# Performance work log

Hardware: AMD Instinct MI355X
Metric: run time of the kernel (lower is better)

The kernel has to match this reference:

```python
import jax, jax.numpy as jnp
import numpy as np

N, E, MUL, NZ, NR = 8192, 65536, 64, 10, 8
SQ3 = 3.0 ** 0.5
SQ2 = 2.0 ** 0.5


def _mlp(x, ws):
    # e3nn FullyConnectedNet: no biases, 1/sqrt(fan_in) scaling, silu on hidden layers
    for i, w in enumerate(ws):
        x = x @ w / jnp.sqrt(jnp.float32(w.shape[0]))
        if i < len(ws) - 1:
            x = jax.nn.silu(x)
    return x


def setup_inputs() -> dict:
    key = jax.random.key(0)
    ks = jax.random.split(key, 20)
    g = lambda i, sh: jax.random.normal(ks[i], sh, dtype=jnp.float32)
    return dict(
        node_attrs=jax.random.uniform(ks[0], (N, NZ), dtype=jnp.float32),
        node_feats=g(1, (N, MUL * 4)),            # 64x0e + 64x1o
        edge_attrs=g(2, (E, 4)),                  # SH: 1x0e + 1x1o
        edge_feats=g(3, (E, NR)),                 # radial basis
        edge_index=jax.random.randint(ks[4], (2, E), 0, N),
        magmom_node_inv_feats=g(5, (N, NR)),
        magmom_node_attrs=g(6, (N, 4)),           # 1x0e + 1x1o
        W_up_s=g(7, (MUL, MUL)), W_up_v=g(8, (MUL, MUL)),
        rmlp_w0=g(9, (2 * NR, 64)), rmlp_w1=g(10, (64, 64)),
        rmlp_w2=g(11, (64, 64)), rmlp_w3=g(12, (64, 5 * MUL)),
        mag_w=g(13, (2 * NR, 13 * MUL)),
        dens_w=g(14, (NR, 1)),
        lin_s_w=g(15, (5 * MUL, MUL)), lin_v_w=g(16, (8 * MUL, MUL)),
        skip_w_s=g(17, (MUL, NZ, MUL)), skip_w_v=g(18, (MUL, NZ, MUL)),
    )


def reference(node_attrs, node_feats, edge_attrs, edge_feats, edge_index,
              magmom_node_inv_feats, magmom_node_attrs,
              W_up_s, W_up_v, rmlp_w0, rmlp_w1, rmlp_w2, rmlp_w3,
              mag_w, dens_w, lin_s_w, lin_v_w, skip_w_s, skip_w_v):
    sender, receiver = edge_index[0], edge_index[1]
    num_nodes = node_feats.shape[0]
    mul = W_up_s.shape[0]

    # linear_up (per-l channel mixing)
    s = node_feats[:, :mul]
    v = node_feats[:, mul:].reshape(num_nodes, mul, 3)
    s = (s @ W_up_s) / jnp.sqrt(jnp.float32(mul))
    v = jnp.einsum('nui,uw->nwi', v, W_up_v) / jnp.sqrt(jnp.float32(mul))

    # radial weights conditioned on edge feats + sender magmom invariants
    efm = jnp.concatenate([edge_feats, magmom_node_inv_feats[sender]], axis=-1)
    tp_w = _mlp(efm, [rmlp_w0, rmlp_w1, rmlp_w2, rmlp_w3]).reshape(-1, 5, mul)
    wm = (efm @ mag_w / jnp.sqrt(jnp.float32(mag_w.shape[0]))).reshape(-1, 13, mul)
    edge_density = jnp.tanh((edge_feats @ dens_w / jnp.sqrt(jnp.float32(NR))) ** 2)  # [E,1]

    # conv_tp: node_feats[sender] x edge SH, uvu with per-edge weights (5 paths)
    xs, xv = s[sender], v[sender]          # [E,mul], [E,mul,3]
    y0, y1 = edge_attrs[:, :1], edge_attrs[:, 1:]
    m_s0 = tp_w[:, 0] * xs * y0                                       # 0e x 0e -> 0e
    m_v0 = tp_w[:, 1, :, None] * xs[:, :, None] * y1[:, None, :]      # 0e x 1o -> 1o
    m_v1 = tp_w[:, 2, :, None] * xv * y0[:, :, None]                  # 1o x 0e -> 1o
    m_s1 = tp_w[:, 3] * jnp.einsum('eui,ei->eu', xv, y1) / SQ3        # 1o x 1o -> 0e
    m_v2 = tp_w[:, 4, :, None] * jnp.cross(xv, y1[:, None, :]) / SQ2  # 1o x 1o -> 1e

    # magmom_conv_tp: mji x magmom_node_attrs[sender], uvu (13 paths)
    ma = magmom_node_attrs[sender]
    m0, m1 = ma[:, :1], ma[:, 1:]
    out_s, out_v = [], []
    p = 0
    for ss in (m_s0, m_s1):
        out_s.append(wm[:, p] * ss * m0); p += 1
        out_v.append(wm[:, p, :, None] * ss[:, :, None] * m1[:, None, :]); p += 1
    for vv in (m_v0, m_v1, m_v2):
        out_v.append(wm[:, p, :, None] * vv * m0[:, :, None]); p += 1
        out_s.append(wm[:, p] * jnp.einsum('eui,ei->eu', vv, m1) / SQ3); p += 1
        out_v.append(wm[:, p, :, None] * jnp.cross(vv, m1[:, None, :]) / SQ2); p += 1
    mm_s = jnp.stack(out_s, axis=1)   # [E,5,mul]
    mm_v = jnp.stack(out_v, axis=1)   # [E,8,mul,3]

    # scatter-sum to receivers
    density = jax.ops.segment_sum(edge_density, receiver, num_segments=num_nodes)  # [N,1]
    ms = jax.ops.segment_sum(mm_s, receiver, num_segments=num_nodes)               # [N,5,mul]
    mv = jax.ops.segment_sum(mm_v, receiver, num_segments=num_nodes)               # [N,8,mul,3]

    # magmom_linear + density normalization
    ms = ms.reshape(num_nodes, 5 * mul) @ lin_s_w / jnp.sqrt(jnp.float32(5 * mul))
    mv = jnp.einsum('nui,uw->nwi', mv.reshape(num_nodes, 8 * mul, 3), lin_v_w) / jnp.sqrt(jnp.float32(8 * mul))
    ms = ms / (density + 1.0)
    mv = mv / (density[:, :, None] + 1.0)

    # skip FullyConnectedTensorProduct with scalar node_attrs (species one-hot)
    fan = jnp.sqrt(jnp.float32(skip_w_s.shape[0] * skip_w_s.shape[1]))
    o_s = jnp.einsum('nu,nv,uvw->nw', ms, node_attrs, skip_w_s) / fan
    o_v = jnp.einsum('nui,nv,uvw->nwi', mv, node_attrs, skip_w_v) / fan

    # reshape_irreps: [N, mul, 1+3]
    return jnp.concatenate([o_s[:, :, None], o_v], axis=-1)
```

## Files before the change

### kernel.cpp

```cpp
#include <hip/hip_runtime.h>
#include <hip/hip_bf16.h>

#define NN 8192
#define EE 65536

typedef unsigned short u16;
typedef __attribute__((ext_vector_type(8))) short bf16x8;
typedef __attribute__((ext_vector_type(8))) unsigned short u16x8;
typedef __attribute__((ext_vector_type(4))) float f32x4;

#define OFF_W0    0
#define OFF_W1    2048
#define OFF_W2    6144
#define OFF_W3M   10240
#define OFF_MAGB  59392
#define OFF_LINS  79872
#define OFF_LINV  100352
#define OFF_SKS   133120
#define OFF_SKV   174080
#define WT_TOTAL  215040

__device__ __forceinline__ u16 f2bf(float f) {
  __hip_bfloat16 h = __float2bfloat16(f);
  return *reinterpret_cast<u16*>(&h);
}
__device__ __forceinline__ float bf2f(u16 v) {
  union { unsigned int u; float f; } x; x.u = ((unsigned int)v) << 16; return x.f;
}
__device__ __forceinline__ void split2(float x, u16& h, u16& l) {
  __hip_bfloat16 bh = __float2bfloat16(x);
  h = *reinterpret_cast<u16*>(&bh);
  float r = x - __bfloat162float(bh);
  __hip_bfloat16 bl = __float2bfloat16(r);
  l = *reinterpret_cast<u16*>(&bl);
}

#define MFMA(a, b, c) __builtin_amdgcn_mfma_f32_16x16x32_bf16((a), (b), (c), 0, 0, 0)

__global__ __launch_bounds__(256, 4) void k_edge(
    const u16* __restrict__ efm_h, const u16* __restrict__ efm_l,
    const u16* __restrict__ wt_h, const u16* __restrict__ wt_l,
    u16* __restrict__ cmbP)
{
  __shared__ u16 Hh[64 * 72], Hl[64 * 72];
  __shared__ u16 Bs[2][3072];
  __shared__ u16 Ct[64 * 80];
  const int tid  = threadIdx.x;
  const size_t pos0 = (size_t)blockIdx.x * 64;
  const int wave = tid >> 6, lane = tid & 63;
  const int quad = lane >> 4, lrow = lane & 15;
  const int kbase = quad * 8;
  const int rw = wave * 16;

  bf16x8 eah = {}, eal = {};
  if (quad < 2) {
    eah = *reinterpret_cast<const bf16x8*>(&efm_h[(pos0 + rw + lrow) * 16 + kbase]);
    eal = *reinterpret_cast<const bf16x8*>(&efm_l[(pos0 + rw + lrow) * 16 + kbase]);
  }

  {
    #pragma unroll
    for (int nt = 0; nt < 4; ++nt) {
      const size_t bo = (size_t)nt * 512 + lane * 8;
      const bf16x8 fbh = *reinterpret_cast<const bf16x8*>(wt_h + OFF_W0 + bo);
      const bf16x8 fbl = *reinterpret_cast<const bf16x8*>(wt_l + OFF_W0 + bo);
      f32x4 acc = {};
      acc = MFMA(eah, fbh, acc); acc = MFMA(eah, fbl, acc); acc = MFMA(eal, fbh, acc);
      #pragma unroll
      for (int r = 0; r < 4; ++r) {
        float t = acc[r];
        t = t / (1.0f + __expf(-t));
        u16 hh, ll; split2(t, hh, ll);
        const int row = rw + quad * 4 + r, col = nt * 16 + lrow;
        Hh[row * 72 + col] = hh; Hl[row * 72 + col] = ll;
      }
    }
  }

  #pragma unroll
  for (int layer = 0; layer < 2; ++layer) {
    const int OFF = layer ? OFF_W2 : OFF_W1;
    bf16x8 fah[2], fal[2];
    #pragma unroll
    for (int ks = 0; ks < 2; ++ks) {
      fah[ks] = *reinterpret_cast<const bf16x8*>(&Hh[(rw + lrow) * 72 + ks * 32 + kbase]);
      fal[ks] = *reinterpret_cast<const bf16x8*>(&Hl[(rw + lrow) * 72 + ks * 32 + kbase]);
    }
    f32x4 acc[4] = {};
    #pragma unroll
    for (int nt = 0; nt < 4; ++nt)
      #pragma unroll
      for (int ks = 0; ks < 2; ++ks) {
        const size_t bo = (size_t)(nt * 2 + ks) * 512 + lane * 8;
        const bf16x8 fbh = *reinterpret_cast<const bf16x8*>(wt_h + OFF + bo);
        const bf16x8 fbl = *reinterpret_cast<const bf16x8*>(wt_l + OFF + bo);
        acc[nt] = MFMA(fah[ks], fbh, acc[nt]);
        acc[nt] = MFMA(fah[ks], fbl, acc[nt]);
        acc[nt] = MFMA(fal[ks], fbh, acc[nt]);
      }
    #pragma unroll
    for (int nt = 0; nt < 4; ++nt)
      #pragma unroll
      for (int r = 0; r < 4; ++r) {
        float t = acc[nt][r];
        t = t / (1.0f + __expf(-t));
        u16 hh, ll; split2(t, hh, ll);
        const int row = rw + quad * 4 + r, col = nt * 16 + lrow;
        Hh[row * 72 + col] = hh; Hl[row * 72 + col] = ll;
      }
  }

  unsigned int tp[5][4][2];

  auto STORE_P = [&](u16* dst) {
    #pragma unroll
    for (int i = 0; i < 2; ++i) {
      const int idx = lane + i * 64;
      const int rl = idx >> 3, c2 = idx & 7;
      const uint4 v4 = *reinterpret_cast<const uint4*>(
          &Ct[(rw + rl) * 80 + ((c2 * 8) ^ (((rl >> 2) & 3) << 4))]);
      *reinterpret_cast<uint4*>(&dst[(pos0 + rw + rl) * 64 + c2 * 8]) = v4;
    }
  };

  {
    bf16x8 fah[3], fal[3];
    #pragma unroll
    for (int ks = 0; ks < 2; ++ks) {
      fah[ks] = *reinterpret_cast<const bf16x8*>(&Hh[(rw + lrow) * 72 + ks * 32 + kbase]);
      fal[ks] = *reinterpret_cast<const bf16x8*>(&Hl[(rw + lrow) * 72 + ks * 32 + kbase]);
    }
    fah[2] = eah; fal[2] = eal;

    auto STAGE_A = [&](int s, int buf) {
      const size_t src = (size_t)OFF_W3M + (size_t)s * 1536;
      #pragma unroll
      for (int i = 0; i < 2; ++i) {
        const int idx = tid + i * 256;
        if (idx < 384) {
          const int b = (idx >= 192);
          const int off = (idx - (b ? 192 : 0)) * 8;
          *reinterpret_cast<uint4*>(&Bs[buf][(b ? 1536 : 0) + off]) =
              *reinterpret_cast<const uint4*>((b ? wt_l : wt_h) + src + off);
        }
      }
    };

    STAGE_A(0, 0);
    #pragma unroll
    for (int s = 0; s < 32; ++s) {
      __syncthreads();
      if (s + 1 < 32) STAGE_A(s + 1, (s + 1) & 1);
      const int nt = s & 3, g = s >> 2;
      f32x4 acc = {};
      #pragma unroll
      for (int ks = 0; ks < 3; ++ks) {
        const bf16x8 bh = *reinterpret_cast<const bf16x8*>(&Bs[s & 1][ks * 512 + lane * 8]);
        const bf16x8 bl = *reinterpret_cast<const bf16x8*>(&Bs[s & 1][1536 + ks * 512 + lane * 8]);
        acc = MFMA(fah[ks], bh, acc); acc = MFMA(fah[ks], bl, acc); acc = MFMA(fal[ks], bh, acc);
      }
      if (g < 5) {
        tp[g][nt][0] = (unsigned)f2bf(acc[0]) | ((unsigned)f2bf(acc[1]) << 16);
        tp[g][nt][1] = (unsigned)f2bf(acc[2]) | ((unsigned)f2bf(acc[3]) << 16);
      } else {
        const int q = (g == 7) ? 3 : 0;
        #pragma unroll
        for (int r = 0; r < 4; ++r) {
          const float tv = bf2f((u16)((tp[q][nt][r >> 1] >> ((r & 1) * 16)) & 0xffffu));
          Ct[(rw + quad * 4 + r) * 80 + ((nt * 16 + lrow) ^ (quad << 4))] = f2bf(acc[r] * tv);
        }
        if (nt == 3) STORE_P(cmbP + (size_t)(g - 5) * ((size_t)EE * 64));
      }
    }
  }

  {
    auto STAGE_B = [&](int t, int buf) {
      const size_t src = (size_t)OFF_MAGB + (size_t)t * 512;
      if (tid < 128) {
        const int b = (tid >= 64);
        const int off = (tid - (b ? 64 : 0)) * 8;
        *reinterpret_cast<uint4*>(&Bs[buf][(b ? 1536 : 0) + off]) =
            *reinterpret_cast<const uint4*>((b ? wt_l : wt_h) + src + off);
      }
    };

    STAGE_B(0, 0);
    #pragma unroll
    for (int t = 0; t < 40; ++t) {
      __syncthreads();
      if (t + 1 < 40) STAGE_B(t + 1, (t + 1) & 1);
      const int nt = t & 3, p = t >> 2;
      constexpr int QB[10] = {3, 1, 1, 1, 2, 2, 2, 4, 4, 4};
      const int q = QB[p];
      const bf16x8 bh = *reinterpret_cast<const bf16x8*>(&Bs[t & 1][lane * 8]);
      const bf16x8 bl = *reinterpret_cast<const bf16x8*>(&Bs[t & 1][1536 + lane * 8]);
      f32x4 acc = {};
      acc = MFMA(eah, bh, acc); acc = MFMA(eah, bl, acc); acc = MFMA(eal, bh, acc);
      #pragma unroll
      for (int r = 0; r < 4; ++r) {
        const float tv = bf2f((u16)((tp[q][nt][r >> 1] >> ((r & 1) * 16)) & 0xffffu));
        Ct[(rw + quad * 4 + r) * 80 + ((nt * 16 + lrow) ^ (quad << 4))] = f2bf(acc[r] * tv);
      }
      if (nt == 3) STORE_P(cmbP + (size_t)(3 + p) * ((size_t)EE * 64));
    }
  }
}

template<int RT, int OUT, bool SILU, int DDIV>
__global__ __launch_bounds__(256) void k_mgemm(
    const u16* __restrict__ X1h, const u16* __restrict__ X1l, int x1rs, int K1,
    const u16* __restrict__ X2h, const u16* __restrict__ X2l, int x2rs, int K2,
    const u16* __restrict__ Wth, const u16* __restrict__ Wtl, int K,
    void* __restrict__ O1, void* __restrict__ O2, int ors,
    const float* __restrict__ dens)
{
  constexpr int NTN = (RT == 128) ? 4 : 1;
  constexpr int AIT = RT * 8 / 256;
  __shared__ u16 Ah[RT * 40];
  __shared__ u16 Al[RT * 40];
  __shared__ u16 Bh[64 * 40];
  __shared__ u16 Bl[64 * 40];
  const int tid  = threadIdx.x;
  const int row0 = blockIdx.x * RT;
  const int col0 = blockIdx.y * 64;
  const int wave = tid >> 6, lane = tid & 63;
  const int quad = lane >> 4, lrow = lane & 15;
  const int kbase = quad * 8;
  const int rw  = (RT == 128) ? wave * 32 : 0;
  const int ntb = (RT == 128) ? 0 : wave;

  f32x4 acc[2][NTN] = {};

  for (int k0 = 0; k0 < K; k0 += 32) {
    #pragma unroll
    for (int i = 0; i < AIT; ++i) {
      const int idx = tid + i * 256;
      const int b = idx / (RT * 4), rc = idx & (RT * 4 - 1);
      const int r = rc >> 2, c = rc & 3;
      const int gk = k0 + c * 8;
      uint4 v = make_uint4(0u, 0u, 0u, 0u);
      if (gk < K1)
        v = *reinterpret_cast<const uint4*>(&(b ? X1l : X1h)[(size_t)(row0 + r) * x1rs + gk]);
      else if (gk - K1 < K2)
        v = *reinterpret_cast<const uint4*>(&(b ? X2l : X2h)[(size_t)(row0 + r) * x2rs + gk - K1]);
      *reinterpret_cast<uint4*>(&(b ? Al : Ah)[r * 40 + c * 8]) = v;
    }
    #pragma unroll
    for (int i = 0; i < 2; ++i) {
      const int idx = tid + i * 256;
      const int b = idx >> 8, rc = idx & 255;
      const int n = rc >> 2, c = rc & 3;
      const uint4 v = *reinterpret_cast<const uint4*>(
          &(b ? Wtl : Wth)[(size_t)(col0 + n) * K + k0 + c * 8]);
      *reinterpret_cast<uint4*>(&(b ? Bl : Bh)[n * 40 + c * 8]) = v;
    }
    __syncthreads();

    bf16x8 fah[2], fal[2], fbh[NTN], fbl[NTN];
    #pragma unroll
    for (int mt = 0; mt < 2; ++mt) {
      const int ro = (rw + mt * 16 + lrow) * 40 + kbase;
      fah[mt] = *reinterpret_cast<const bf16x8*>(&Ah[ro]);
      fal[mt] = *reinterpret_cast<const bf16x8*>(&Al[ro]);
    }
    #pragma unroll
    for (int nt = 0; nt < NTN; ++nt) {
      const int ro = ((ntb + nt) * 16 + lrow) * 40 + kbase;
      fbh[nt] = *reinterpret_cast<const bf16x8*>(&Bh[ro]);
      fbl[nt] = *reinterpret_cast<const bf16x8*>(&Bl[ro]);
    }
    #pragma unroll
    for (int mt = 0; mt < 2; ++mt)
      #pragma unroll
      for (int nt = 0; nt < NTN; ++nt) {
        acc[mt][nt] = MFMA(fah[mt], fbh[nt], acc[mt][nt]);
        acc[mt][nt] = MFMA(fah[mt], fbl[nt], acc[mt][nt]);
        acc[mt][nt] = MFMA(fal[mt], fbh[nt], acc[mt][nt]);
      }
    __syncthreads();
  }

  #pragma unroll
  for (int mt = 0; mt < 2; ++mt)
    #pragma unroll
    for (int nt = 0; nt < NTN; ++nt)
      #pragma unroll
      for (int r = 0; r < 4; ++r) {
        const int grow = row0 + rw + mt * 16 + quad * 4 + r;
        const int gcol = col0 + (ntb + nt) * 16 + lrow;
        float t = acc[mt][nt][r];
        if (SILU) t = t / (1.0f + __expf(-t));
        if (DDIV > 0) t *= 1.0f / (dens[grow / DDIV] + 1.0f);
        const size_t oi = (size_t)grow * ors + gcol;
        if (OUT == 0) {
          reinterpret_cast<float*>(O1)[oi] = t;
        } else if (OUT == 1) {
          u16 hh, ll;
          split2(t, hh, ll);
          reinterpret_cast<u16*>(O1)[oi] = hh;
          reinterpret_cast<u16*>(O2)[oi] = ll;
        } else {
          reinterpret_cast<u16*>(O1)[oi] = f2bf(t);
        }
      }
}

__global__ __launch_bounds__(256) void k_skipm(
    const float* __restrict__ ms2, const float* __restrict__ mv2,
    const float* __restrict__ na,
    const u16* __restrict__ wt_h, const u16* __restrict__ wt_l,
    float* __restrict__ out)
{
  __shared__ u16 Ah[32 * 40];
  __shared__ u16 Al[32 * 40];
  __shared__ u16 Bh[64 * 40];
  __shared__ u16 Bl[64 * 40];
  const int tid  = threadIdx.x;
  const bool isv = blockIdx.x >= (NN / 32);
  const int row0 = (isv ? (blockIdx.x - NN / 32) : blockIdx.x) * 32;
  const float* C = isv ? mv2 : ms2;
  const u16* Bth = wt_h + (isv ? OFF_SKV : OFF_SKS);
  const u16* Btl = wt_l + (isv ? OFF_SKV : OFF_SKS);
  const int wave = tid >> 6, lane = tid & 63;
  const int quad = lane >> 4, lrow = lane & 15;
  const int kbase = quad * 8;

  f32x4 acc[2] = {};

  for (int k0 = 0; k0 < 640; k0 += 32) {
    #pragma unroll
    for (int i = 0; i < 4; ++i) {
      const int e = tid + i * 256;
      const int r = e >> 5, kk = e & 31;
      const int k = k0 + kk;
      const int u = k / 10, v = k - u * 10;
      const int row = row0 + r;
      const int n = isv ? (row / 3) : row;
      const float t = C[(size_t)row * 64 + u] * na[n * 10 + v];
      u16 hh, ll;
      split2(t, hh, ll);
      Ah[r * 40 + kk] = hh;
      Al[r * 40 + kk] = ll;
    }
    #pragma unroll
    for (int i = 0; i < 2; ++i) {
      const int idx = tid + i * 256;
      const int b = idx >> 8, rc = idx & 255;
      const int nw = rc >> 2, c = rc & 3;
      const uint4 v4 = *reinterpret_cast<const uint4*>(
          &(b ? Btl : Bth)[(size_t)nw * 640 + k0 + c * 8]);
      *reinterpret_cast<uint4*>(&(b ? Bl : Bh)[nw * 40 + c * 8]) = v4;
    }
    __syncthreads();

    bf16x8 fah[2], fal[2], fbh, fbl;
    #pragma unroll
    for (int mt = 0; mt < 2; ++mt) {
      const int ro = (mt * 16 + lrow) * 40 + kbase;
      fah[mt] = *reinterpret_cast<const bf16x8*>(&Ah[ro]);
      fal[mt] = *reinterpret_cast<const bf16x8*>(&Al[ro]);
    }
    {
      const int ro = (wave * 16 + lrow) * 40 + kbase;
      fbh = *reinterpret_cast<const bf16x8*>(&Bh[ro]);
      fbl = *reinterpret_cast<const bf16x8*>(&Bl[ro]);
    }
    #pragma unroll
    for (int mt = 0; mt < 2; ++mt) {
      acc[mt] = MFMA(fah[mt], fbh, acc[mt]);
      acc[mt] = MFMA(fah[mt], fbl, acc[mt]);
      acc[mt] = MFMA(fal[mt], fbh, acc[mt]);
    }
    __syncthreads();
  }

  #pragma unroll
  for (int mt = 0; mt < 2; ++mt)
    #pragma unroll
    for (int r = 0; r < 4; ++r) {
      const int row = row0 + mt * 16 + quad * 4 + r;
      const int w = wave * 16 + lrow;
      if (isv) {
        const int n = row / 3, i = row - n * 3;
        out[(size_t)n * 256 + w * 4 + 1 + i] = acc[mt][r];
      } else {
        out[(size_t)row * 256 + w * 4] = acc[mt][r];
      }
    }
}

template<int RT>
__global__ __launch_bounds__(256) void k_gemm(
    const float* __restrict__ X, int xrs, int xes, int xco, int xcob,
    const float* __restrict__ W, int K, int NOUT,
    float scale, float* __restrict__ OUTp, int ors, int oob)
{
  constexpr int RPT = RT / 16;
  __shared__ float Xs[RT * 65];
  __shared__ float Ws[64 * 64];
  const int tid  = threadIdx.x;
  const int row0 = blockIdx.x * RT;
  const int col0 = blockIdx.y * 64;
  const int z    = blockIdx.z;
  const int xc   = xco + z * xcob;
  const int oo   = z * oob;
  const int ci = tid & 15;
  const int ri = tid >> 4;
  float acc[RPT][4] = {};

  for (int k0 = 0; k0 < K; k0 += 64) {
    const int kc  = (K - k0 >= 64) ? 64 : (K - k0);
    const int ksh = (kc == 64) ? 6 : 4;
    for (int idx = tid; idx < kc * RT; idx += 256) {
      const int r = idx >> ksh, kk = idx & (kc - 1);
      Xs[r * 65 + kk] = X[(size_t)(row0 + r) * xrs + xc + (size_t)(k0 + kk) * xes];
    }
    for (int idx = tid; idx < (kc << 6); idx += 256) {
      const int kk = idx >> 6, c = idx & 63;
      Ws[kk * 64 + c] = W[(size_t)(k0 + kk) * NOUT + col0 + c];
    }
    __syncthreads();
    for (int kk = 0; kk < kc; ++kk) {
      const float4 wv = *reinterpret_cast<const float4*>(&Ws[kk * 64 + ci * 4]);
      #pragma unroll
      for (int j = 0; j < RPT; ++j) {
        const float x = Xs[(ri * RPT + j) * 65 + kk];
        acc[j][0] += x * wv.x; acc[j][1] += x * wv.y;
        acc[j][2] += x * wv.z; acc[j][3] += x * wv.w;
      }
    }
    __syncthreads();
  }

  #pragma unroll
  for (int j = 0; j < RPT; ++j) {
    const int row = row0 + ri * RPT + j;
    *reinterpret_cast<float4*>(OUTp + (size_t)row * ors + oo + col0 + ci * 4) =
        make_float4(acc[j][0] * scale, acc[j][1] * scale, acc[j][2] * scale, acc[j][3] * scale);
  }
}

__global__ __launch_bounds__(256) void k_count(const int* __restrict__ rcv, int* __restrict__ counts) {
  const int e = blockIdx.x * 256 + threadIdx.x;
  atomicAdd(&counts[rcv[e]], 1);
}

__global__ __launch_bounds__(1024) void k_scan(const int* __restrict__ counts,
                                               int* __restrict__ offs, int* __restrict__ cursor) {
  __shared__ int part[1024];
  const int tid = threadIdx.x;
  int local[8];
  int s = 0;
  #pragma unroll
  for (int j = 0; j < 8; ++j) { local[j] = s; s += counts[tid * 8 + j]; }
  part[tid] = s;
  __syncthreads();
  for (int off = 1; off < 1024; off <<= 1) {
    int v = 0;
    if (tid >= off) v = part[tid - off];
    __syncthreads();
    part[tid] += v;
    __syncthreads();
  }
  const int base = part[tid] - s;
  #pragma unroll
  for (int j = 0; j < 8; ++j) {
    const int o = base + local[j];
    offs[tid * 8 + j] = o;
    cursor[tid * 8 + j] = o;
  }
  if (tid == 1023) offs[NN] = part[1023];
}

__global__ __launch_bounds__(256) void k_fill(const int* __restrict__ rcv,
                                              int* __restrict__ cursor, int* __restrict__ perm) {
  const int e = blockIdx.x * 256 + threadIdx.x;
  const int pos = atomicAdd(&cursor[rcv[e]], 1);
  perm[pos] = e;
}

__global__ __launch_bounds__(256) void k_permw(
    const float* __restrict__ w0, const float* __restrict__ w1,
    const float* __restrict__ w2, const float* __restrict__ w3,
    const float* __restrict__ mag_w, const float* __restrict__ lin_s,
    const float* __restrict__ lin_v, const float* __restrict__ skip_s,
    const float* __restrict__ skip_v,
    u16* __restrict__ wt_h, u16* __restrict__ wt_l)
{
  const int id = blockIdx.x * 256 + threadIdx.x;
  float val = 0.f;
  if (id < OFF_W1) {
    const int i = id - OFF_W0;
    const int tile = i >> 9, rem = i & 511, lane = rem >> 3, e = rem & 7;
    const int quad = lane >> 4, lrow = lane & 15;
    const int n = tile * 16 + lrow, k = quad * 8 + e;
    val = (k < 16) ? w0[k * 64 + n] * 0.25f : 0.f;
  } else if (id < OFF_W2) {
    const int i = id - OFF_W1;
    const int tile = i >> 9, rem = i & 511, lane = rem >> 3, e = rem & 7;
    const int quad = lane >> 4, lrow = lane & 15;
    const int n = (tile >> 1) * 16 + lrow, k = (tile & 1) * 32 + quad * 8 + e;
    val = w1[k * 64 + n] * 0.125f;
  } else if (id < OFF_W3M) {
    const int i = id - OFF_W2;
    const int tile = i >> 9, rem = i & 511, lane = rem >> 3, e = rem & 7;
    const int quad = lane >> 4, lrow = lane & 15;
    const int n = (tile >> 1) * 16 + lrow, k = (tile & 1) * 32 + quad * 8 + e;
    val = w2[k * 64 + n] * 0.125f;
  } else if (id < OFF_MAGB) {
    const int i = id - OFF_W3M;
    const int tile = i >> 9, rem = i & 511, lane = rem >> 3, e = rem & 7;
    const int quad = lane >> 4, lrow = lane & 15;
    const int gnt = tile / 3, ks = tile - gnt * 3;
    const int n = (gnt >> 2) * 64 + (gnt & 3) * 16 + lrow;
    const int k = ks * 32 + quad * 8 + e;
    if (n < 320) {
      val = (k < 64) ? w3[k * 320 + n] * 0.125f : 0.f;
    } else {
      const int p = (n - 320) >> 6, u = n & 63;
      val = (k >= 64 && k < 80) ? mag_w[(k - 64) * 832 + p * 64 + u] * 0.25f : 0.f;
    }
  } else if (id < OFF_LINS) {
    const int i = id - OFF_MAGB;
    const int tile = i >> 9, rem = i & 511, lane = rem >> 3, e = rem & 7;
    const int quad = lane >> 4, lrow = lane & 15;
    const int n = (tile >> 2) * 64 + (tile & 3) * 16 + lrow;
    const int k = quad * 8 + e;
    const int p = n >> 6, u = n & 63;
    val = (k < 16) ? mag_w[k * 832 + (3 + p) * 64 + u] * 0.25f : 0.f;
  } else if (id < OFF_LINV) {
    const int i = id - OFF_LINS, n = i / 320, k = i - n * 320;
    val = lin_s[k * 64 + n] * 0.05590169944f;
  } else if (id < OFF_SKS) {
    const int i = id - OFF_LINV, n = i >> 9, k = i & 511;
    val = lin_v[k * 64 + n] * 0.04419417382f;
  } else if (id < OFF_SKV) {
    const int i = id - OFF_SKS, w = i / 640, k = i - w * 640;
    val = skip_s[k * 64 + w] * 0.03952847075f;
  } else if (id < WT_TOTAL) {
    const int i = id - OFF_SKV, w = i / 640, k = i - w * 640;
    val = skip_v[k * 64 + w] * 0.03952847075f;
  } else {
    return;
  }
  u16 hh, ll;
  split2(val, hh, ll);
  wt_h[id] = hh;
  wt_l[id] = ll;
}

__global__ __launch_bounds__(256) void k_build(
    const int* __restrict__ perm, const int* __restrict__ snd,
    const float* __restrict__ edge_attrs, const float* __restrict__ edge_feats,
    const float* __restrict__ mm_inv, const float* __restrict__ dens_w,
    int* __restrict__ snd_perm, float* __restrict__ ya_perm,
    float* __restrict__ dq_perm, u16* __restrict__ efm_h, u16* __restrict__ efm_l)
{
  const int pos = blockIdx.x * 256 + threadIdx.x;
  const int e = perm[pos];
  const int s = snd[e];
  snd_perm[pos] = s;
  reinterpret_cast<float4*>(ya_perm)[pos] = reinterpret_cast<const float4*>(edge_attrs)[e];
  const float4 ef0 = reinterpret_cast<const float4*>(edge_feats)[e * 2];
  const float4 ef1 = reinterpret_cast<const float4*>(edge_feats)[e * 2 + 1];
  const float4 mi0 = reinterpret_cast<const float4*>(mm_inv)[s * 2];
  const float4 mi1 = reinterpret_cast<const float4*>(mm_inv)[s * 2 + 1];
  float q = ef0.x * dens_w[0] + ef0.y * dens_w[1] + ef0.z * dens_w[2] + ef0.w * dens_w[3]
          + ef1.x * dens_w[4] + ef1.y * dens_w[5] + ef1.z * dens_w[6] + ef1.w * dens_w[7];
  q *= 0.35355339059f;
  dq_perm[pos] = tanhf(q * q);
  float vals[16] = { ef0.x, ef0.y, ef0.z, ef0.w, ef1.x, ef1.y, ef1.z, ef1.w,
                     mi0.x, mi0.y, mi0.z, mi0.w, mi1.x, mi1.y, mi1.z, mi1.w };
  u16 hh[16], ll[16];
  #pragma unroll
  for (int i = 0; i < 16; ++i) split2(vals[i], hh[i], ll[i]);
  reinterpret_cast<uint4*>(&efm_h[(size_t)pos * 16])[0] = reinterpret_cast<uint4*>(hh)[0];
  reinterpret_cast<uint4*>(&efm_h[(size_t)pos * 16])[1] = reinterpret_cast<uint4*>(hh)[1];
  reinterpret_cast<uint4*>(&efm_l[(size_t)pos * 16])[0] = reinterpret_cast<uint4*>(ll)[0];
  reinterpret_cast<uint4*>(&efm_l[(size_t)pos * 16])[1] = reinterpret_cast<uint4*>(ll)[1];
}

__global__ __launch_bounds__(256) void k_gather(
    const int* __restrict__ snd_perm,
    const float* __restrict__ ya_perm,
    const float* __restrict__ dq_perm,
    const float* __restrict__ mm_attrs,
    const float* __restrict__ s_buf,
    const float* __restrict__ v_buf,
    const u16* __restrict__ cmbP,
    const int* __restrict__ offs,
    u16* __restrict__ ms_h, u16* __restrict__ ms_l,
    u16* __restrict__ mv_h, u16* __restrict__ mv_l,
    float* __restrict__ dens)
{
  __shared__ float red[2][30][64];
  const int tid  = threadIdx.x;
  const int lane = tid & 63;
  const int nib  = tid >> 7;
  const int half = (tid >> 6) & 1;
  const int n = blockIdx.x * 2 + nib;

  float acc_s[5] = {0.f, 0.f, 0.f, 0.f, 0.f};
  float acc_v[8][3] = {};
  float dacc = 0.f;
  const int start0 = offs[n], end0 = offs[n + 1];
  const int mid = start0 + ((end0 - start0 + 1) >> 1);
  const int start = half ? mid : start0;
  const int end   = half ? end0 : mid;

  int s_nx = 0;
  if (start < end) s_nx = snd_perm[start];
  for (int pos = start; pos < end; ++pos) {
    const int s = s_nx;
    if (pos + 1 < end) s_nx = snd_perm[pos + 1];

    const float4 ya = reinterpret_cast<const float4*>(ya_perm)[pos];
    const float4 mm = reinterpret_cast<const float4*>(mm_attrs)[s];
    dacc += dq_perm[pos];
    const float y0 = ya.x, y1x = ya.y, y1y = ya.z, y1z = ya.w;
    const float m0 = mm.x, m1x = mm.y, m1y = mm.z, m1z = mm.w;
    const float xs  = s_buf[s * 64 + lane];
    const float xvx = v_buf[(s * 3 + 0) * 64 + lane];
    const float xvy = v_buf[(s * 3 + 1) * 64 + lane];
    const float xvz = v_buf[(s * 3 + 2) * 64 + lane];

    float cp[13];
    #pragma unroll
    for (int p = 0; p < 13; ++p)
      cp[p] = bf2f(cmbP[(size_t)p * ((size_t)EE * 64) + (size_t)pos * 64 + lane]);

    const float gs0 = xs * y0;
    const float gd  = (xvx * y1x + xvy * y1y + xvz * y1z) * 0.57735026919f;
    const float g0x = xs * y1x, g0y = xs * y1y, g0z = xs * y1z;
    const float g1x = xvx * y0, g1y = xvy * y0, g1z = xvz * y0;
    const float g2x = (xvy * y1z - xvz * y1y) * 0.70710678119f;
    const float g2y = (xvz * y1x - xvx * y1z) * 0.70710678119f;
    const float g2z = (xvx * y1y - xvy * y1x) * 0.70710678119f;

    acc_s[0]    += cp[0] * gs0 * m0;
    acc_v[0][0] += cp[1] * gs0 * m1x; acc_v[0][1] += cp[1] * gs0 * m1y; acc_v[0][2] += cp[1] * gs0 * m1z;
    acc_s[1]    += cp[2] * gd * m0;
    acc_v[1][0] += cp[3] * gd * m1x; acc_v[1][1] += cp[3] * gd * m1y; acc_v[1][2] += cp[3] * gd * m1z;

#define VV_BLOCK(vx, vy, vz, cA, cB, cC, vslotA, sslot, vslotB)                           \
    acc_v[vslotA][0] += (cA) * (vx) * m0;                                                 \
    acc_v[vslotA][1] += (cA) * (vy) * m0;                                                 \
    acc_v[vslotA][2] += (cA) * (vz) * m0;                                                 \
    acc_s[sslot] += (cB) * ((vx) * m1x + (vy) * m1y + (vz) * m1z) * 0.57735026919f;       \
    {                                                                                     \
      const float ccx = (vy) * m1z - (vz) * m1y;                                          \
      const float ccy = (vz) * m1x - (vx) * m1z;                                          \
      const float ccz = (vx) * m1y - (vy) * m1x;                                          \
      acc_v[vslotB][0] += (cC) * ccx * 0.70710678119f;                                    \
      acc_v[vslotB][1] += (cC) * ccy * 0.70710678119f;                                    \
      acc_v[vslotB][2] += (cC) * ccz * 0.70710678119f;                                    \
    }

    VV_BLOCK(g0x, g0y, g0z, cp[4], cp[5], cp[6], 2, 2, 3)
    VV_BLOCK(g1x, g1y, g1z, cp[7], cp[8], cp[9], 4, 3, 5)
    VV_BLOCK(g2x, g2y, g2z, cp[10], cp[11], cp[12], 6, 4, 7)
#undef VV_BLOCK
  }

  if (half == 1) {
    #pragma unroll
    for (int j = 0; j < 5; ++j) red[nib][j][lane] = acc_s[j];
    #pragma unroll
    for (int p = 0; p < 8; ++p)
      #pragma unroll
      for (int i = 0; i < 3; ++i) red[nib][5 + p * 3 + i][lane] = acc_v[p][i];
    red[nib][29][lane] = dacc;
  }
  __syncthreads();
  if (half == 0) {
    #pragma unroll
    for (int j = 0; j < 5; ++j) acc_s[j] += red[nib][j][lane];
    #pragma unroll
    for (int p = 0; p < 8; ++p)
      #pragma unroll
      for (int i = 0; i < 3; ++i) acc_v[p][i] += red[nib][5 + p * 3 + i][lane];
    dacc += red[nib][29][lane];

    #pragma unroll
    for (int j = 0; j < 5; ++j) {
      u16 hh, ll;
      split2(acc_s[j], hh, ll);
      ms_h[(size_t)n * 320 + j * 64 + lane] = hh;
      ms_l[(size_t)n * 320 + j * 64 + lane] = ll;
    }
    #pragma unroll
    for (int p = 0; p < 8; ++p)
      #pragma unroll
      for (int i = 0; i < 3; ++i) {
        u16 hh, ll;
        split2(acc_v[p][i], hh, ll);
        mv_h[((size_t)n * 3 + i) * 512 + p * 64 + lane] = hh;
        mv_l[((size_t)n * 3 + i) * 512 + p * 64 + lane] = ll;
      }
    if (lane == 0) dens[n] = dacc;
  }
}

extern "C" void kernel_launch(void* const* d_in, const int* in_sizes, int n_in,
                              void* d_out, int out_size, void* d_ws, size_t ws_size,
                              hipStream_t stream)
{
  const float* node_attrs = (const float*)d_in[0];
  const float* node_feats = (const float*)d_in[1];
  const float* edge_attrs = (const float*)d_in[2];
  const float* edge_feats = (const float*)d_in[3];
  const int*   edge_index = (const int*)d_in[4];
  const float* mm_inv     = (const float*)d_in[5];
  const float* mm_attrs   = (const float*)d_in[6];
  const float* W_up_s     = (const float*)d_in[7];
  const float* W_up_v     = (const float*)d_in[8];
  const float* w0         = (const float*)d_in[9];
  const float* w1         = (const float*)d_in[10];
  const float* w2         = (const float*)d_in[11];
  const float* w3         = (const float*)d_in[12];
  const float* mag_w      = (const float*)d_in[13];
  const float* dens_w     = (const float*)d_in[14];
  const float* lin_s      = (const float*)d_in[15];
  const float* lin_v      = (const float*)d_in[16];
  const float* skip_s     = (const float*)d_in[17];
  const float* skip_v     = (const float*)d_in[18];
  float* out = (float*)d_out;

  char* wp = (char*)d_ws;
  auto alloc = [&](size_t b) { char* p = wp; wp += (b + 255) & ~(size_t)255; return p; };
  float* s_buf  = (float*)alloc((size_t)NN * 64 * 4);
  float* v_buf  = (float*)alloc((size_t)NN * 192 * 4);
  float* ya_p   = (float*)alloc((size_t)EE * 4 * 4);
  float* dq_p   = (float*)alloc((size_t)EE * 4);
  int*   snd_p  = (int*)alloc((size_t)EE * 4);
  u16*   efm_h  = (u16*)alloc((size_t)EE * 16 * 2);
  u16*   efm_l  = (u16*)alloc((size_t)EE * 16 * 2);
  u16*   hA_h   = (u16*)alloc((size_t)EE * 64 * 2);
  u16*   hA_l   = (u16*)alloc((size_t)EE * 64 * 2);
  u16*   hB_h   = (u16*)alloc((size_t)EE * 64 * 2);
  u16*   hB_l   = (u16*)alloc((size_t)EE * 64 * 2);
  u16*   cmbP   = (u16*)alloc((size_t)13 * EE * 64 * 2);
  u16*   mv_h   = (u16*)alloc((size_t)NN * 1536 * 2);
  u16*   mv_l   = (u16*)alloc((size_t)NN * 1536 * 2);
  float* dens   = (float*)alloc((size_t)NN * 4);
  int*   counts = (int*)alloc((size_t)NN * 4);
  int*   offs   = (int*)alloc((size_t)(NN + 1) * 4);
  int*   cursor = (int*)alloc((size_t)NN * 4);
  int*   perm   = (int*)alloc((size_t)EE * 4);
  u16*   wt_h   = (u16*)alloc((size_t)WT_TOTAL * 2);
  u16*   wt_l   = (u16*)alloc((size_t)WT_TOTAL * 2);
  u16*   ms_h   = hB_h;
  u16*   ms_l   = hB_l;
  float* ms2    = (float*)hA_h;
  float* mv2    = (float*)hA_l;

  const int* snd = edge_index;
  const int* rcv = edge_index + EE;

  hipMemsetAsync(counts, 0, (size_t)NN * 4, stream);
  k_count<<<EE / 256, 256, 0, stream>>>(rcv, counts);
  k_scan<<<1, 1024, 0, stream>>>(counts, offs, cursor);
  k_fill<<<EE / 256, 256, 0, stream>>>(rcv, cursor, perm);
  k_build<<<EE / 256, 256, 0, stream>>>(perm, snd, edge_attrs, edge_feats, mm_inv, dens_w,
                                        snd_p, ya_p, dq_p, efm_h, efm_l);
  k_permw<<<(WT_TOTAL + 255) / 256, 256, 0, stream>>>(w0, w1, w2, w3, mag_w, lin_s, lin_v,
                                                     skip_s, skip_v, wt_h, wt_l);

  k_gemm<32><<<dim3(NN / 32, 1, 1), 256, 0, stream>>>(
      node_feats, 256, 1, 0, 0, W_up_s, 64, 64, 0.125f, s_buf, 64, 0);
  k_gemm<32><<<dim3(NN / 32, 1, 3), 256, 0, stream>>>(
      node_feats, 256, 3, 64, 1, W_up_v, 64, 64, 0.125f, v_buf, 192, 64);

  k_edge<<<EE / 64, 256, 0, stream>>>(efm_h, efm_l, wt_h, wt_l, cmbP);

  k_gather<<<NN / 2, 256, 0, stream>>>(snd_p, ya_p, dq_p, mm_attrs,
                                       s_buf, v_buf, cmbP, offs,
                                       ms_h, ms_l, mv_h, mv_l, dens);

  k_mgemm<32, 0, false, 1><<<dim3(NN / 32, 1), 256, 0, stream>>>(
      ms_h, ms_l, 320, 320, nullptr, nullptr, 0, 0,
      wt_h + OFF_LINS, wt_l + OFF_LINS, 320, ms2, nullptr, 64, dens);
  k_mgemm<32, 0, false, 3><<<dim3(NN * 3 / 32, 1), 256, 0, stream>>>(
      mv_h, mv_l, 512, 512, nullptr, nullptr, 0, 0,
      wt_h + OFF_LINV, wt_l + OFF_LINV, 512, mv2, nullptr, 64, dens);

  k_skipm<<<NN / 32 + NN * 3 / 32, 256, 0, stream>>>(
      ms2, mv2, node_attrs, wt_h, wt_l, out);
}
```

Measured before the change: 296.5 us.

## Interleave radial and magmom GEMM phases to shrink tp register array

Merges the two GEMM phases (radial MLP last layer and magmom projection) into one table-driven loop over 18 product tiles. Each tp group is consumed right after it is computed, so only a 4x2 register buffer is kept instead of 5x4x2. This cuts register pressure and may raise occupancy. In exchange, the outer loop is no longer unrolled and uses runtime lookups in device constant tables, which adds branching and scalar loads.

```diff
diff --git a/kernel.cpp b/kernel.cpp
--- a/kernel.cpp
+++ b/kernel.cpp
@@ -19,6 +19,10 @@
 #define OFF_SKS   133120
 #define OFF_SKV   174080
 #define WT_TOTAL  215040
+
+__device__ const int PKIND[18] = {0,0,0, 0,0,1, 0,1,1,1, 0,1,1,1, 0,1,1,1};
+__device__ const int PTILE[18] = {0,5,6, 3,7,0, 1,1,2,3, 2,4,5,6, 4,7,8,9};
+__device__ const int PROLE[18] = {-1,0,1, -1,2,3, -1,4,5,6, -1,7,8,9, -1,10,11,12};
 
 __device__ __forceinline__ u16 f2bf(float f) {
   __hip_bfloat16 h = __float2bfloat16(f);
@@ -110,19 +114,6 @@
       }
   }
 
-  unsigned int tp[5][4][2];
-
-  auto STORE_P = [&](u16* dst) {
-    #pragma unroll
-    for (int i = 0; i < 2; ++i) {
-      const int idx = lane + i * 64;
-      const int rl = idx >> 3, c2 = idx & 7;
-      const uint4 v4 = *reinterpret_cast<const uint4*>(
-          &Ct[(rw + rl) * 80 + ((c2 * 8) ^ (((rl >> 2) & 3) << 4))]);
-      *reinterpret_cast<uint4*>(&dst[(pos0 + rw + rl) * 64 + c2 * 8]) = v4;
-    }
-  };
-
   {
     bf16x8 fah[3], fal[3];
     #pragma unroll
@@ -132,77 +123,77 @@
     }
     fah[2] = eah; fal[2] = eal;
 
-    auto STAGE_A = [&](int s, int buf) {
-      const size_t src = (size_t)OFF_W3M + (size_t)s * 1536;
-      #pragma unroll
-      for (int i = 0; i < 2; ++i) {
-        const int idx = tid + i * 256;
-        if (idx < 384) {
-          const int b = (idx >= 192);
-          const int off = (idx - (b ? 192 : 0)) * 8;
+    auto STAGE = [&](int pl, int nt, int buf) {
+      if (PKIND[pl]) {
+        const size_t src = (size_t)OFF_MAGB + (size_t)(PTILE[pl] * 4 + nt) * 512;
+        if (tid < 128) {
+          const int b = (tid >= 64);
+          const int off = (tid - (b ? 64 : 0)) * 8;
           *reinterpret_cast<uint4*>(&Bs[buf][(b ? 1536 : 0) + off]) =
               *reinterpret_cast<const uint4*>((b ? wt_l : wt_h) + src + off);
         }
+      } else {
+        const size_t src = (size_t)OFF_W3M + (size_t)(PTILE[pl] * 4 + nt) * 1536;
+        #pragma unroll
+        for (int i2 = 0; i2 < 2; ++i2) {
+          const int idx = tid + i2 * 256;
+          if (idx < 384) {
+            const int b = (idx >= 192);
+            const int off = (idx - (b ? 192 : 0)) * 8;
+            *reinterpret_cast<uint4*>(&Bs[buf][(b ? 1536 : 0) + off]) =
+                *reinterpret_cast<const uint4*>((b ? wt_l : wt_h) + src + off);
+          }
+        }
       }
     };
 
-    STAGE_A(0, 0);
-    #pragma unroll
-    for (int s = 0; s < 32; ++s) {
-      __syncthreads();
-      if (s + 1 < 32) STAGE_A(s + 1, (s + 1) & 1);
-      const int nt = s & 3, g = s >> 2;
-      f32x4 acc = {};
-      #pragma unroll
-      for (int ks = 0; ks < 3; ++ks) {
-        const bf16x8 bh = *reinterpret_cast<const bf16x8*>(&Bs[s & 1][ks * 512 + lane * 8]);
-        const bf16x8 bl = *reinterpret_cast<const bf16x8*>(&Bs[s & 1][1536 + ks * 512 + lane * 8]);
-        acc = MFMA(fah[ks], bh, acc); acc = MFMA(fah[ks], bl, acc); acc = MFMA(fal[ks], bh, acc);
-      }
-      if (g < 5) {
-        tp[g][nt][0] = (unsigned)f2bf(acc[0]) | ((unsigned)f2bf(acc[1]) << 16);
-        tp[g][nt][1] = (unsigned)f2bf(acc[2]) | ((unsigned)f2bf(acc[3]) << 16);
-      } else {
-        const int q = (g == 7) ? 3 : 0;
-        #pragma unroll
-        for (int r = 0; r < 4; ++r) {
-          const float tv = bf2f((u16)((tp[q][nt][r >> 1] >> ((r & 1) * 16)) & 0xffffu));
-          Ct[(rw + quad * 4 + r) * 80 + ((nt * 16 + lrow) ^ (quad << 4))] = f2bf(acc[r] * tv);
+    auto STORE_P = [&](u16* dst) {
+      #pragma unroll
+      for (int i = 0; i < 2; ++i) {
+        const int idx = lane + i * 64;
+        const int rl = idx >> 3, c2 = idx & 7;
+        const uint4 v4 = *reinterpret_cast<const uint4*>(
+            &Ct[(rw + rl) * 80 + ((c2 * 8) ^ (((rl >> 2) & 3) << 4))]);
+        *reinterpret_cast<uint4*>(&dst[(pos0 + rw + rl) * 64 + c2 * 8]) = v4;
+      }
+    };
+
+    unsigned int tp[4][2];
+    int buf = 0;
+    STAGE(0, 0, 0);
+    for (int pl = 0; pl < 18; ++pl) {
+      const int kind = PKIND[pl], role = PROLE[pl];
+      #pragma unroll
+      for (int nt = 0; nt < 4; ++nt) {
+        __syncthreads();
+        if (nt < 3) STAGE(pl, nt + 1, buf ^ 1);
+        else if (pl + 1 < 18) STAGE(pl + 1, 0, buf ^ 1);
+        f32x4 acc = {};
+        if (kind == 0) {
+          #pragma unroll
+          for (int ks = 0; ks < 3; ++ks) {
+            const bf16x8 bh = *reinterpret_cast<const bf16x8*>(&Bs[buf][ks * 512 + lane * 8]);
+            const bf16x8 bl = *reinterpret_cast<const bf16x8*>(&Bs[buf][1536 + ks * 512 + lane * 8]);
+            acc = MFMA(fah[ks], bh, acc); acc = MFMA(fah[ks], bl, acc); acc = MFMA(fal[ks], bh, acc);
+          }
+        } else {
+          const bf16x8 bh = *reinterpret_cast<const bf16x8*>(&Bs[buf][lane * 8]);
+          const bf16x8 bl = *reinterpret_cast<const bf16x8*>(&Bs[buf][1536 + lane * 8]);
+          acc = MFMA(fah[2], bh, acc); acc = MFMA(fah[2], bl, acc); acc = MFMA(fal[2], bh, acc);
         }
-        if (nt == 3) STORE_P(cmbP + (size_t)(g - 5) * ((size_t)EE * 64));
-      }
-    }
-  }
-
-  {
-    auto STAGE_B = [&](int t, int buf) {
-      const size_t src = (size_t)OFF_MAGB + (size_t)t * 512;
-      if (tid < 128) {
-        const int b = (tid >= 64);
-        const int off = (tid - (b ? 64 : 0)) * 8;
-        *reinterpret_cast<uint4*>(&Bs[buf][(b ? 1536 : 0) + off]) =
-            *reinterpret_cast<const uint4*>((b ? wt_l : wt_h) + src + off);
-      }
-    };
-
-    STAGE_B(0, 0);
-    #pragma unroll
-    for (int t = 0; t < 40; ++t) {
-      __syncthreads();
-      if (t + 1 < 40) STAGE_B(t + 1, (t + 1) & 1);
-      const int nt = t & 3, p = t >> 2;
-      constexpr int QB[10] = {3, 1, 1, 1, 2, 2, 2, 4, 4, 4};
-      const int q = QB[p];
-      const bf16x8 bh = *reinterpret_cast<const bf16x8*>(&Bs[t & 1][lane * 8]);
-      const bf16x8 bl = *reinterpret_cast<const bf16x8*>(&Bs[t & 1][1536 + lane * 8]);
-      f32x4 acc = {};
-      acc = MFMA(eah, bh, acc); acc = MFMA(eah, bl, acc); acc = MFMA(eal, bh, acc);
-      #pragma unroll
-      for (int r = 0; r < 4; ++r) {
-        const float tv = bf2f((u16)((tp[q][nt][r >> 1] >> ((r & 1) * 16)) & 0xffffu));
-        Ct[(rw + quad * 4 + r) * 80 + ((nt * 16 + lrow) ^ (quad << 4))] = f2bf(acc[r] * tv);
-      }
-      if (nt == 3) STORE_P(cmbP + (size_t)(3 + p) * ((size_t)EE * 64));
+        if (role < 0) {
+          tp[nt][0] = (unsigned)f2bf(acc[0]) | ((unsigned)f2bf(acc[1]) << 16);
+          tp[nt][1] = (unsigned)f2bf(acc[2]) | ((unsigned)f2bf(acc[3]) << 16);
+        } else {
+          #pragma unroll
+          for (int r = 0; r < 4; ++r) {
+            const float tv = bf2f((u16)((tp[nt][r >> 1] >> ((r & 1) * 16)) & 0xffffu));
+            Ct[(rw + quad * 4 + r) * 80 + ((nt * 16 + lrow) ^ (quad << 4))] = f2bf(acc[r] * tv);
+          }
+        }
+        buf ^= 1;
+      }
+      if (role >= 0) STORE_P(cmbP + (size_t)role * ((size_t)EE * 64));
     }
   }
 }
```

Measured after the change: 290.7 us. About the same (-2.0%).
